# Performance work log

Measured on AMD Instinct MI355X. Metric: run time of the kernel, lower is better.

The kernel has to match this reference:

```python
import jax, jax.numpy as jnp
import numpy as np

N = 4096  # out_features (rows of W)
M = 4096  # in_features (cols of W)
S = 2048  # number of Givens pairs per side (= N//2)
TOKENS = 2048
EPS = 1e-8


def setup_inputs() -> dict:
    key = jax.random.key(0)
    ks = jax.random.split(key, 6)
    x = jax.random.normal(ks[0], (TOKENS, M), dtype=jnp.float32)
    W = jax.random.normal(ks[1], (N, M), dtype=jnp.float32) * (1.0 / np.sqrt(M))
    bias = jax.random.normal(ks[2], (N,), dtype=jnp.float32) * 0.02
    theta_L = 0.02 * jax.random.normal(ks[3], (S,), dtype=jnp.float32)
    theta_R = 0.02 * jax.random.normal(ks[4], (S,), dtype=jnp.float32)
    ecd_log_mag = jnp.zeros((N,), dtype=jnp.float32)
    # disjoint index pairs: (0,1),(2,3),... as produced by a permutation reshape
    pairs_L = jnp.arange(N, dtype=jnp.int64).reshape(S, 2)
    pairs_R = jnp.arange(M, dtype=jnp.int64).reshape(S, 2)
    return {"x": x, "W": W, "bias": bias, "theta_L": theta_L,
            "theta_R": theta_R, "ecd_log_mag": ecd_log_mag,
            "pairs_L": pairs_L, "pairs_R": pairs_R}


def _apply_left_rotations(W, theta, pairs):
    # Plane (Givens) rotations on disjoint row pairs of W: [S] angles, [S,2] indices
    c = jnp.cos(theta)[:, None]
    s = jnp.sin(theta)[:, None]
    i, j = pairs[:, 0], pairs[:, 1]
    ri, rj = W[i], W[j]                       # [S, M] gathers
    return W.at[i].set(c * ri - s * rj).at[j].set(s * ri + c * rj)


def _apply_right_rotations(W, theta, pairs):
    # Plane rotations on disjoint column pairs of W
    c = jnp.cos(theta)
    s = jnp.sin(theta)
    p, q = pairs[:, 0], pairs[:, 1]
    cp, cq = W[:, p], W[:, q]                 # [N, S] gathers
    return W.at[:, p].set(c * cp - s * cq).at[:, q].set(s * cp + c * cq)


def reference(x, W, bias, theta_L, theta_R, ecd_log_mag, pairs_L, pairs_R):
    # base row norms are buffers computed under no_grad from the frozen base weight
    base_row_norms = jax.lax.stop_gradient(jnp.linalg.norm(W, axis=1))  # [N]
    Wp = _apply_left_rotations(W, theta_L, pairs_L)
    Wp = _apply_right_rotations(Wp, theta_R, pairs_R)
    # magnitude rescale: row-normalize rotated weight, scale by learned magnitude
    row_norm = jnp.linalg.norm(Wp, axis=1, keepdims=True)               # [N,1]
    mag = base_row_norms * jnp.exp(ecd_log_mag)                         # [N]
    W_eff = Wp * (mag[:, None] / (row_norm + EPS))                      # [N,M]
    return x @ W_eff.T + bias                                           # [T,N]
```

## Files before the change

kernel.cpp:

```cpp
#include <hip/hip_runtime.h>
#include <hip/hip_bf16.h>


#define GK 4096
#define GN 4096
#define GT 2048
#define NPAIR 2048

typedef __bf16 bf16x8 __attribute__((ext_vector_type(8)));
typedef float  f32x4  __attribute__((ext_vector_type(4)));

static __device__ __forceinline__ unsigned short f2bf(float f) {
    union { float f; unsigned int u; } v; v.f = f;
    unsigned int r = v.u + 0x7fffu + ((v.u >> 16) & 1u);
    return (unsigned short)(r >> 16);
}
static __device__ __forceinline__ unsigned int pack2bf(float a, float b) {
    return (unsigned int)f2bf(a) | ((unsigned int)f2bf(b) << 16);
}

__global__ __launch_bounds__(256) void prelude(
    const float* __restrict__ W, const float* __restrict__ thL,
    const float* __restrict__ thR, const float* __restrict__ ecd,
    const float* __restrict__ x,
    unsigned short* __restrict__ Weff, unsigned short* __restrict__ Xbf)
{
    const int tid = threadIdx.x;

    if (blockIdx.x >= 2048) {
        const int cb = blockIdx.x - 2048;
        const size_t base = (size_t)cb * 512;
        const float4* X4 = (const float4*)x;
        uint4* O4 = (uint4*)Xbf;
#pragma unroll
        for (int k = 0; k < 2; k++) {
            const size_t m = base + tid + k * 256;
            const float4 a = X4[2 * m];
            const float4 b = X4[2 * m + 1];
            uint4 o;
            o.x = pack2bf(a.x, a.y);
            o.y = pack2bf(a.z, a.w);
            o.z = pack2bf(b.x, b.y);
            o.w = pack2bf(b.z, b.w);
            O4[m] = o;
        }
        return;
    }

    const int s  = blockIdx.x;
    const int i0 = 2 * s, i1 = 2 * s + 1;

    const float tl = thL[s];
    const float cL = cosf(tl), sL = sinf(tl);

    float4 b0[4], b1[4];
    float s00 = 0.f, s11 = 0.f, s01 = 0.f;

    const float4* r0 = (const float4*)(W + (size_t)i0 * GK);
    const float4* r1 = (const float4*)(W + (size_t)i1 * GK);
    const float2* T2 = (const float2*)thR;

#pragma unroll
    for (int k = 0; k < 4; k++) {
        const int c4 = tid + k * 256;
        const float4 w0 = r0[c4];
        const float4 w1 = r1[c4];
        const float2 tt = T2[c4];
        float4 cs;
        sincosf(tt.x, &cs.y, &cs.x);
        sincosf(tt.y, &cs.w, &cs.z);
        s00 += w0.x * w0.x + w0.y * w0.y + w0.z * w0.z + w0.w * w0.w;
        s11 += w1.x * w1.x + w1.y * w1.y + w1.z * w1.z + w1.w * w1.w;
        s01 += w0.x * w1.x + w0.y * w1.y + w0.z * w1.z + w0.w * w1.w;
        const float a0x = cL * w0.x - sL * w1.x;
        const float a0y = cL * w0.y - sL * w1.y;
        const float a0z = cL * w0.z - sL * w1.z;
        const float a0w = cL * w0.w - sL * w1.w;
        const float a1x = sL * w0.x + cL * w1.x;
        const float a1y = sL * w0.y + cL * w1.y;
        const float a1z = sL * w0.z + cL * w1.z;
        const float a1w = sL * w0.w + cL * w1.w;
        b0[k].x = cs.x * a0x - cs.y * a0y;
        b0[k].y = cs.y * a0x + cs.x * a0y;
        b0[k].z = cs.z * a0z - cs.w * a0w;
        b0[k].w = cs.w * a0z + cs.z * a0w;
        b1[k].x = cs.x * a1x - cs.y * a1y;
        b1[k].y = cs.y * a1x + cs.x * a1y;
        b1[k].z = cs.z * a1z - cs.w * a1w;
        b1[k].w = cs.w * a1z + cs.z * a1w;
    }

#pragma unroll
    for (int off = 32; off; off >>= 1) {
        s00 += __shfl_down(s00, off);
        s11 += __shfl_down(s11, off);
        s01 += __shfl_down(s01, off);
    }
    __shared__ float red[3][4];
    __shared__ float scales[2];
    const int wave = tid >> 6, lane = tid & 63;
    if (lane == 0) { red[0][wave] = s00; red[1][wave] = s11; red[2][wave] = s01; }
    __syncthreads();
    if (tid == 0) {
        const float t0 = red[0][0] + red[0][1] + red[0][2] + red[0][3];
        const float t1 = red[1][0] + red[1][1] + red[1][2] + red[1][3];
        const float td = red[2][0] + red[2][1] + red[2][2] + red[2][3];
        const float n0 = cL * cL * t0 + sL * sL * t1 - 2.f * cL * sL * td;
        const float n1 = sL * sL * t0 + cL * cL * t1 + 2.f * cL * sL * td;
        scales[0] = sqrtf(t0) * expf(ecd[i0]) / (sqrtf(n0) + 1e-8f);
        scales[1] = sqrtf(t1) * expf(ecd[i1]) / (sqrtf(n1) + 1e-8f);
    }
    __syncthreads();
    const float sc0 = scales[0], sc1 = scales[1];

    uint2* o0 = (uint2*)(Weff + (size_t)i0 * GK);
    uint2* o1 = (uint2*)(Weff + (size_t)i1 * GK);
#pragma unroll
    for (int k = 0; k < 4; k++) {
        const int c4 = tid + k * 256;
        uint2 p0, p1;
        p0.x = pack2bf(b0[k].x * sc0, b0[k].y * sc0);
        p0.y = pack2bf(b0[k].z * sc0, b0[k].w * sc0);
        p1.x = pack2bf(b1[k].x * sc1, b1[k].y * sc1);
        p1.y = pack2bf(b1[k].z * sc1, b1[k].w * sc1);
        o0[c4] = p0;
        o1[c4] = p1;
    }
}

static __device__ __forceinline__ void glds16(const unsigned short* g, unsigned short* l) {
    __builtin_amdgcn_global_load_lds(
        (const __attribute__((address_space(1))) unsigned int*)g,
        (__attribute__((address_space(3))) unsigned int*)l, 16, 0, 0);
}

__global__ __launch_bounds__(256, 2) void gemm_bt(
    const unsigned short* __restrict__ A,
    const unsigned short* __restrict__ B,
    const float* __restrict__ bias,
    float* __restrict__ C)
{
    constexpr int BM = 128, BN = 128, BK = 64;
    constexpr int NT = GK / BK;
    __shared__ unsigned short smem[2][2][BM * BK];

    const int tid  = threadIdx.x;
    const int lane = tid & 63;
    const int wave = tid >> 6;
    const int quad = lane >> 4;
    const int l16  = lane & 15;
    const int wm   = wave >> 1;
    const int wn   = wave & 1;
    const int bm   = blockIdx.y * BM;
    const int bn   = blockIdx.x * BN;

    const int lrow = lane >> 3;
    const int jlog = (lane & 7) ^ lrow;
    const unsigned short* gA[4];
    const unsigned short* gB[4];
    int loff[4];
#pragma unroll
    for (int j = 0; j < 4; j++) {
        const int chunk = j * 4 + wave;
        gA[j] = A + (size_t)(bm + chunk * 8 + lrow) * GK + jlog * 8;
        gB[j] = B + (size_t)(bn + chunk * 8 + lrow) * GK + jlog * 8;
        loff[j] = chunk * 512 + lane * 8;
    }

#define STAGE(buf, k0) do {                                               \
    _Pragma("unroll")                                                     \
    for (int j = 0; j < 4; j++) {                                         \
        glds16(gA[j] + (k0), &smem[buf][0][loff[j]]);                     \
        glds16(gB[j] + (k0), &smem[buf][1][loff[j]]);                     \
    } } while (0)

    f32x4 acc[4][4] = {};

#define COMPUTE(b) do {                                                   \
    const unsigned short* As_ = &smem[b][0][0];                           \
    const unsigned short* Bs_ = &smem[b][1][0];                           \
    bf16x8 aF[2][4], bF[2][4];                                            \
    _Pragma("unroll")                                                     \
    for (int kk = 0; kk < 2; kk++) {                                      \
        _Pragma("unroll")                                                 \
        for (int i = 0; i < 4; i++) {                                     \
            const int ps = ((quad + 4 * kk) ^ (l16 & 7)) * 8;             \
            aF[kk][i] = *(const bf16x8*)(As_ + (wm * 64 + i * 16 + l16) * BK + ps); \
            bF[kk][i] = *(const bf16x8*)(Bs_ + (wn * 64 + i * 16 + l16) * BK + ps); \
        } }                                                               \
    _Pragma("unroll")                                                     \
    for (int i = 0; i < 4; i++) {                                         \
        _Pragma("unroll")                                                 \
        for (int j = 0; j < 4; j++) {                                     \
            acc[i][j] = __builtin_amdgcn_mfma_f32_16x16x32_bf16(          \
                aF[0][i], bF[0][j], acc[i][j], 0, 0, 0);                  \
            acc[i][j] = __builtin_amdgcn_mfma_f32_16x16x32_bf16(          \
                aF[1][i], bF[1][j], acc[i][j], 0, 0, 0);                  \
        } }                                                               \
    } while (0)

    STAGE(0, 0);
    int cur = 0;
    for (int t = 0; t < NT - 1; ++t) {
        STAGE(cur ^ 1, (t + 1) * BK);
        __builtin_amdgcn_sched_barrier(0);
        asm volatile("s_waitcnt vmcnt(8)" ::: "memory");
        __builtin_amdgcn_s_barrier();
        __builtin_amdgcn_sched_barrier(0);
        COMPUTE(cur);
        __builtin_amdgcn_sched_barrier(0);
        __builtin_amdgcn_s_barrier();
        cur ^= 1;
    }
    asm volatile("s_waitcnt vmcnt(0)" ::: "memory");
    __builtin_amdgcn_s_barrier();
    __builtin_amdgcn_sched_barrier(0);
    COMPUTE(cur);

#undef STAGE
#undef COMPUTE

#pragma unroll
    for (int i = 0; i < 4; i++) {
        const int m = bm + wm * 64 + i * 16 + quad * 4;
#pragma unroll
        for (int j = 0; j < 4; j++) {
            const int n = bn + wn * 64 + j * 16 + l16;
            const float bv = bias[n];
#pragma unroll
            for (int r = 0; r < 4; r++)
                C[(size_t)(m + r) * GN + n] = acc[i][j][r] + bv;
        }
    }
}

extern "C" void kernel_launch(void* const* d_in, const int* in_sizes, int n_in,
                              void* d_out, int out_size, void* d_ws, size_t ws_size,
                              hipStream_t stream) {
    const float* x    = (const float*)d_in[0];
    const float* W    = (const float*)d_in[1];
    const float* bias = (const float*)d_in[2];
    const float* thL  = (const float*)d_in[3];
    const float* thR  = (const float*)d_in[4];
    const float* ecd  = (const float*)d_in[5];

    unsigned short* Weff = (unsigned short*)d_ws;
    unsigned short* Xbf  = (unsigned short*)((char*)d_ws + (size_t)GN * GK * 2);

    float* out = (float*)d_out;

    prelude<<<dim3(4096), dim3(256), 0, stream>>>(W, thL, thR, ecd, x, Weff, Xbf);
    gemm_bt<<<dim3(GN / 128, GT / 128), dim3(256), 0, stream>>>(Xbf, Weff, bias, out);
}
```

Before: 208.7 us.

## Load A fragments directly into registers, stage only B through LDS

Result: slower. 277.4 us (+32.9%).

```diff
diff --git a/kernel.cpp b/kernel.cpp
--- a/kernel.cpp
+++ b/kernel.cpp
@@ -142,7 +142,7 @@
 {
     constexpr int BM = 128, BN = 128, BK = 64;
     constexpr int NT = GK / BK;
-    __shared__ unsigned short smem[2][2][BM * BK];
+    __shared__ unsigned short Bs[2][BN * BK];
 
     const int tid  = threadIdx.x;
     const int lane = tid & 63;
@@ -156,69 +156,106 @@
 
     const int lrow = lane >> 3;
     const int jlog = (lane & 7) ^ lrow;
-    const unsigned short* gA[4];
     const unsigned short* gB[4];
-    int loff[4];
+    int loffB[4];
 #pragma unroll
     for (int j = 0; j < 4; j++) {
-        const int chunk = j * 4 + wave;
-        gA[j] = A + (size_t)(bm + chunk * 8 + lrow) * GK + jlog * 8;
-        gB[j] = B + (size_t)(bn + chunk * 8 + lrow) * GK + jlog * 8;
-        loff[j] = chunk * 512 + lane * 8;
-    }
-
-#define STAGE(buf, k0) do {                                               \
-    _Pragma("unroll")                                                     \
-    for (int j = 0; j < 4; j++) {                                         \
-        glds16(gA[j] + (k0), &smem[buf][0][loff[j]]);                     \
-        glds16(gB[j] + (k0), &smem[buf][1][loff[j]]);                     \
+        const int c = j * 4 + wave;
+        gB[j] = B + (size_t)(bn + c * 8 + lrow) * GK + jlog * 8;
+        loffB[j] = c * 512 + lane * 8;
+    }
+
+    const unsigned short* Arow[4];
+#pragma unroll
+    for (int i = 0; i < 4; i++)
+        Arow[i] = A + (size_t)(bm + wm * 64 + i * 16 + l16) * GK + quad * 8;
+
+#define STAGE_B(buf, k0) do {                                             \
+    _Pragma("unroll")                                                     \
+    for (int j = 0; j < 4; j++)                                           \
+        glds16(gB[j] + (k0), &Bs[buf][loffB[j]]);                         \
+    } while (0)
+
+#define A_LOADS(dst, k0) do {                                             \
+    _Pragma("unroll")                                                     \
+    for (int i = 0; i < 4; i++) {                                         \
+        asm volatile("global_load_dwordx4 %0, %1, off"                    \
+            : "=&v"(dst[0][i]) : "v"(Arow[i] + (k0)));                    \
+        asm volatile("global_load_dwordx4 %0, %1, off"                    \
+            : "=&v"(dst[1][i]) : "v"(Arow[i] + (k0) + 32));               \
     } } while (0)
 
     f32x4 acc[4][4] = {};
 
-#define COMPUTE(b) do {                                                   \
-    const unsigned short* As_ = &smem[b][0][0];                           \
-    const unsigned short* Bs_ = &smem[b][1][0];                           \
-    bf16x8 aF[2][4], bF[2][4];                                            \
+#define COMPUTE(buf, aF) do {                                             \
+    bf16x8 bF[2][4];                                                      \
     _Pragma("unroll")                                                     \
     for (int kk = 0; kk < 2; kk++) {                                      \
+        const int ps = ((quad + 4 * kk) ^ (l16 & 7)) * 8;                 \
         _Pragma("unroll")                                                 \
-        for (int i = 0; i < 4; i++) {                                     \
-            const int ps = ((quad + 4 * kk) ^ (l16 & 7)) * 8;             \
-            aF[kk][i] = *(const bf16x8*)(As_ + (wm * 64 + i * 16 + l16) * BK + ps); \
-            bF[kk][i] = *(const bf16x8*)(Bs_ + (wn * 64 + i * 16 + l16) * BK + ps); \
-        } }                                                               \
-    _Pragma("unroll")                                                     \
-    for (int i = 0; i < 4; i++) {                                         \
+        for (int j = 0; j < 4; j++)                                       \
+            bF[kk][j] = *(const bf16x8*)&Bs[buf][(wn * 64 + j * 16 + l16) * BK + ps]; \
+    }                                                                     \
+    _Pragma("unroll")                                                     \
+    for (int i = 0; i < 4; i++)                                           \
         _Pragma("unroll")                                                 \
         for (int j = 0; j < 4; j++) {                                     \
             acc[i][j] = __builtin_amdgcn_mfma_f32_16x16x32_bf16(          \
                 aF[0][i], bF[0][j], acc[i][j], 0, 0, 0);                  \
             acc[i][j] = __builtin_amdgcn_mfma_f32_16x16x32_bf16(          \
                 aF[1][i], bF[1][j], acc[i][j], 0, 0, 0);                  \
-        } }                                                               \
-    } while (0)
-
-    STAGE(0, 0);
-    int cur = 0;
-    for (int t = 0; t < NT - 1; ++t) {
-        STAGE(cur ^ 1, (t + 1) * BK);
-        __builtin_amdgcn_sched_barrier(0);
-        asm volatile("s_waitcnt vmcnt(8)" ::: "memory");
-        __builtin_amdgcn_s_barrier();
-        __builtin_amdgcn_sched_barrier(0);
-        COMPUTE(cur);
-        __builtin_amdgcn_sched_barrier(0);
-        __builtin_amdgcn_s_barrier();
-        cur ^= 1;
-    }
+        }                                                                 \
+    } while (0)
+
+#define WAIT12_BAR do {                                                   \
+    __builtin_amdgcn_sched_barrier(0);                                    \
+    asm volatile("s_waitcnt vmcnt(12)" ::: "memory");                     \
+    __builtin_amdgcn_sched_barrier(0);                                    \
+    __builtin_amdgcn_s_barrier();                                         \
+    __builtin_amdgcn_sched_barrier(0);                                    \
+    } while (0)
+
+#define END_BAR do {                                                      \
+    __builtin_amdgcn_sched_barrier(0);                                    \
+    __builtin_amdgcn_s_barrier();                                         \
+    } while (0)
+
+    bf16x8 aX[2][4], aY[2][4];
+
+    STAGE_B(0, 0);
+    A_LOADS(aX, 0);
+
+    for (int t = 0; t < NT - 2; t += 2) {
+        STAGE_B(1, (t + 1) * BK);
+        A_LOADS(aY, (t + 1) * BK);
+        WAIT12_BAR;
+        COMPUTE(0, aX);
+        END_BAR;
+
+        STAGE_B(0, (t + 2) * BK);
+        A_LOADS(aX, (t + 2) * BK);
+        WAIT12_BAR;
+        COMPUTE(1, aY);
+        END_BAR;
+    }
+    STAGE_B(1, (NT - 1) * BK);
+    A_LOADS(aY, (NT - 1) * BK);
+    WAIT12_BAR;
+    COMPUTE(0, aX);
+    END_BAR;
+
+    __builtin_amdgcn_sched_barrier(0);
     asm volatile("s_waitcnt vmcnt(0)" ::: "memory");
+    __builtin_amdgcn_sched_barrier(0);
     __builtin_amdgcn_s_barrier();
     __builtin_amdgcn_sched_barrier(0);
-    COMPUTE(cur);
-
-#undef STAGE
+    COMPUTE(1, aY);
+
+#undef STAGE_B
+#undef A_LOADS
 #undef COMPUTE
+#undef WAIT12_BAR
+#undef END_BAR
 
 #pragma unroll
     for (int i = 0; i < 4; i++) {
```
